# Optimization experiments

Measured on AMD Instinct MI355X. Metric: run time of the kernel, lower is better.

The kernel has to match this reference:

```python
import jax, jax.numpy as jnp
import numpy as np

HEADS = 4
HEAD_DIM = 32
IN_DIM = 128
N_TRIG = 48
N_SPAN = 128


def build_edges(T, S):
    # nodes are (trig r, span c) flattened row-major: n = r*S + c
    N = T * S
    nodes = jnp.arange(N, dtype=jnp.int32)
    r = nodes // S
    c = nodes % S
    # same-row neighbors (includes self loop once): [N, S]
    row_nb = r[:, None] * S + jnp.arange(S, dtype=jnp.int32)[None, :]
    # same-column neighbors excluding own row: [N, T-1]
    t_idx = jnp.arange(T - 1, dtype=jnp.int32)[None, :]
    t = t_idx + (t_idx >= r[:, None]).astype(jnp.int32)
    col_nb = t * S + c[:, None]
    deg = S + T - 1
    src = jnp.concatenate([row_nb, col_nb], axis=1).reshape(-1)  # [N*deg]
    dst = jnp.repeat(nodes, deg)
    return src, dst, N


def gat_conv(x, src, dst, N, W, att_src, att_dst, bias):
    # PyG GATConv (eval mode, dropout off), concat=True.
    # W: [in, H*Hd]; att_src/att_dst: [H, Hd]; bias: [H*Hd]
    h = (x @ W).reshape(N, HEADS, HEAD_DIM)          # [N,H,Hd]
    a_src = jnp.sum(h * att_src[None], axis=-1)      # [N,H]
    a_dst = jnp.sum(h * att_dst[None], axis=-1)      # [N,H]
    e = jax.nn.leaky_relu(a_src[src] + a_dst[dst], negative_slope=0.2)  # [E,H]
    # scatter-softmax over incoming edges per destination node
    m = jax.ops.segment_max(e, dst, num_segments=N)  # [N,H]
    ex = jnp.exp(e - m[dst])
    denom = jax.ops.segment_sum(ex, dst, num_segments=N)
    alpha = ex / denom[dst]                          # [E,H]
    msg = alpha[:, :, None] * h[src]                 # [E,H,Hd]
    out = jax.ops.segment_sum(msg, dst, num_segments=N)  # [N,H,Hd]
    return out.reshape(N, HEADS * HEAD_DIM) + bias[None]


def setup_inputs() -> dict:
    key = jax.random.key(0)
    ks = jax.random.split(key, 9)
    D = IN_DIM
    HD = HEADS * HEAD_DIM
    inp = {
        "pair_embeddings": jax.random.normal(ks[0], (1, N_TRIG, N_SPAN, D), dtype=jnp.float32),
        "W1": jax.random.normal(ks[1], (D, HD), dtype=jnp.float32) * (2.0 / (D + HD)) ** 0.5,
        "att_src1": jax.random.normal(ks[2], (HEADS, HEAD_DIM), dtype=jnp.float32) * 0.1,
        "att_dst1": jax.random.normal(ks[3], (HEADS, HEAD_DIM), dtype=jnp.float32) * 0.1,
        "b1": jnp.zeros((HD,), dtype=jnp.float32),
        "W2": jax.random.normal(ks[4], (HD, HD), dtype=jnp.float32) * (2.0 / (HD + HD)) ** 0.5,
        "att_src2": jax.random.normal(ks[5], (HEADS, HEAD_DIM), dtype=jnp.float32) * 0.1,
        "att_dst2": jax.random.normal(ks[6], (HEADS, HEAD_DIM), dtype=jnp.float32) * 0.1,
        "b2": jnp.zeros((HD,), dtype=jnp.float32),
        "num_trigs_kept": N_TRIG,
        "num_arg_spans_kept": N_SPAN,
    }
    return inp


def reference(pair_embeddings, W1, att_src1, att_dst1, b1, W2, att_src2, att_dst2, b2, num_trigs_kept, num_arg_spans_kept):
    T, S = int(num_trigs_kept), int(num_arg_spans_kept)
    src, dst, N = build_edges(T, S)
    # batch_size == 1: slice and flatten node features
    x = pair_embeddings[0, :T, :S].reshape(N, -1)
    x = jax.nn.elu(gat_conv(x, src, dst, N, W1, att_src1, att_dst1, b1))
    x = jax.nn.elu(gat_conv(x, src, dst, N, W2, att_src2, att_dst2, b2))
    return x
```

## Files before the change

kernel.cpp:

```cpp
#include <hip/hip_runtime.h>

#define T_TRIG 48
#define S_SPAN 128
#define NN (T_TRIG * S_SPAN)
#define D 128
#define DEG (S_SPAN + T_TRIG - 1)

__global__ __launch_bounds__(256) void gemm_att_kernel(
    const float* __restrict__ X, const float* __restrict__ W,
    const float* __restrict__ att_s, const float* __restrict__ att_d,
    float* __restrict__ H, float* __restrict__ asrc, float* __restrict__ adst)
{
    __shared__ float wl[128 * 128];
    const int tid = threadIdx.x;
    {
        const float4* W4 = (const float4*)W;
        float4* wl4 = (float4*)wl;
        #pragma unroll
        for (int i = 0; i < 16; ++i)
            wl4[tid + i * 256] = W4[tid + i * 256];
    }
    __syncthreads();

    const int tx = tid & 15;
    const int ty = tid >> 4;
    const int i0 = blockIdx.x * 32 + ty * 2;
    const int j0 = tx * 8;

    float acc[2][8];
    #pragma unroll
    for (int a = 0; a < 2; ++a)
        #pragma unroll
        for (int b = 0; b < 8; ++b) acc[a][b] = 0.f;

    const float* x0 = X + i0 * D;
    for (int k = 0; k < D; k += 4) {
        float4 xa4 = *(const float4*)(x0 + k);
        float4 xb4 = *(const float4*)(x0 + D + k);
        float xa[4] = {xa4.x, xa4.y, xa4.z, xa4.w};
        float xb[4] = {xb4.x, xb4.y, xb4.z, xb4.w};
        #pragma unroll
        for (int kk = 0; kk < 4; ++kk) {
            const float* wr = &wl[(k + kk) * 128 + j0];
            float4 w0 = *(const float4*)(wr);
            float4 w1 = *(const float4*)(wr + 4);
            float wv[8] = {w0.x, w0.y, w0.z, w0.w, w1.x, w1.y, w1.z, w1.w};
            #pragma unroll
            for (int jj = 0; jj < 8; ++jj) {
                acc[0][jj] = fmaf(xa[kk], wv[jj], acc[0][jj]);
                acc[1][jj] = fmaf(xb[kk], wv[jj], acc[1][jj]);
            }
        }
    }

    #pragma unroll
    for (int ii = 0; ii < 2; ++ii) {
        float4 o0 = {acc[ii][0], acc[ii][1], acc[ii][2], acc[ii][3]};
        float4 o1 = {acc[ii][4], acc[ii][5], acc[ii][6], acc[ii][7]};
        *(float4*)&H[(i0 + ii) * D + j0]     = o0;
        *(float4*)&H[(i0 + ii) * D + j0 + 4] = o1;
    }

    const int head = tx >> 2;
    const int dbase = head * 32 + (tx & 3) * 8;
    float asv[8], adv[8];
    #pragma unroll
    for (int jj = 0; jj < 8; ++jj) {
        asv[jj] = att_s[dbase + jj];
        adv[jj] = att_d[dbase + jj];
    }
    #pragma unroll
    for (int ii = 0; ii < 2; ++ii) {
        float ps = 0.f, pd = 0.f;
        #pragma unroll
        for (int jj = 0; jj < 8; ++jj) {
            ps = fmaf(acc[ii][jj], asv[jj], ps);
            pd = fmaf(acc[ii][jj], adv[jj], pd);
        }
        ps += __shfl_xor(ps, 1); ps += __shfl_xor(ps, 2);
        pd += __shfl_xor(pd, 1); pd += __shfl_xor(pd, 2);
        if ((tx & 3) == 0) {
            asrc[(i0 + ii) * 4 + head] = ps;
            adst[(i0 + ii) * 4 + head] = pd;
        }
    }
}

__global__ __launch_bounds__(128) void agg_kernel(
    const float* __restrict__ H, const float4* __restrict__ asrc4,
    const float4* __restrict__ adst4, const float* __restrict__ bias,
    float* __restrict__ out)
{
    __shared__ float w[DEG + 1][4];
    __shared__ float inv_den[4];

    const int tid = threadIdx.x;
    const int n = blockIdx.x;
    const int r = n >> 7;
    const int c = n & 127;

    const float4 ad = adst4[n];
    for (int j = tid; j < DEG; j += 128) {
        int src;
        if (j < 128) {
            src = (r << 7) + j;
        } else {
            int t = j - 128;
            t += (t >= r) ? 1 : 0;
            src = (t << 7) + c;
        }
        float4 as = asrc4[src];
        float e0 = as.x + ad.x; e0 = e0 > 0.f ? e0 : 0.2f * e0;
        float e1 = as.y + ad.y; e1 = e1 > 0.f ? e1 : 0.2f * e1;
        float e2 = as.z + ad.z; e2 = e2 > 0.f ? e2 : 0.2f * e2;
        float e3 = as.w + ad.w; e3 = e3 > 0.f ? e3 : 0.2f * e3;
        float4 ev = {e0, e1, e2, e3};
        *(float4*)&w[j][0] = ev;
    }
    __syncthreads();

    {
        const int head = tid >> 5;
        const int l = tid & 31;
        float m = -1e30f;
        for (int j = l; j < DEG; j += 32) m = fmaxf(m, w[j][head]);
        #pragma unroll
        for (int o = 16; o > 0; o >>= 1) m = fmaxf(m, __shfl_xor(m, o));
        float s = 0.f;
        for (int j = l; j < DEG; j += 32) {
            float v = __expf(w[j][head] - m);
            w[j][head] = v;
            s += v;
        }
        #pragma unroll
        for (int o = 16; o > 0; o >>= 1) s += __shfl_xor(s, o);
        if (l == 0) inv_den[head] = 1.f / s;
    }
    __syncthreads();

    const int f = tid;
    const int head = tid >> 5;
    float acc = 0.f;

    const float* hrow = H + (r << 7) * D + f;
    #pragma unroll 8
    for (int j = 0; j < S_SPAN; ++j)
        acc = fmaf(w[j][head], hrow[j * D], acc);

    const float* hcol = H + c * D + f;
    #pragma unroll 4
    for (int j2 = 0; j2 < T_TRIG - 1; ++j2) {
        int t = j2 + ((j2 >= r) ? 1 : 0);
        acc = fmaf(w[128 + j2][head], hcol[t * (S_SPAN * D)], acc);
    }

    acc = acc * inv_den[head] + bias[f];
    out[n * D + f] = acc > 0.f ? acc : (__expf(acc) - 1.f);
}

extern "C" void kernel_launch(void* const* d_in, const int* in_sizes, int n_in,
                              void* d_out, int out_size, void* d_ws, size_t ws_size,
                              hipStream_t stream)
{
    const float* pe  = (const float*)d_in[0];
    const float* W1  = (const float*)d_in[1];
    const float* as1 = (const float*)d_in[2];
    const float* ad1 = (const float*)d_in[3];
    const float* b1  = (const float*)d_in[4];
    const float* W2  = (const float*)d_in[5];
    const float* as2 = (const float*)d_in[6];
    const float* ad2 = (const float*)d_in[7];
    const float* b2  = (const float*)d_in[8];
    float* out = (float*)d_out;

    char* ws = (char*)d_ws;
    float* H    = (float*)(ws);
    float* X2   = (float*)(ws + (size_t)NN * D * 4);
    float* asrc = (float*)(ws + (size_t)2 * NN * D * 4);
    float* adst = (float*)(ws + (size_t)2 * NN * D * 4 + (size_t)NN * 4 * 4);

    gemm_att_kernel<<<dim3(NN / 32), dim3(256), 0, stream>>>(pe, W1, as1, ad1, H, asrc, adst);
    agg_kernel<<<dim3(NN), dim3(128), 0, stream>>>(H, (const float4*)asrc, (const float4*)adst, b1, X2);
    gemm_att_kernel<<<dim3(NN / 32), dim3(256), 0, stream>>>(X2, W2, as2, ad2, H, asrc, adst);
    agg_kernel<<<dim3(NN), dim3(128), 0, stream>>>(H, (const float4*)asrc, (const float4*)adst, b2, out);
}
```

Baseline: 84.23 us.

## Split GAT aggregation into row and column kernels sharing tiles in LDS

Replaces the per-node aggregation kernel with a row kernel (one block per trigger row and head) and a column kernel (one block per span column). Each stages its H tile once in shared memory and reuses it across all destination nodes, instead of re-gathering neighbor features per node. The softmax drops max-subtraction and combines unnormalized row and column partial sums, which risks exp overflow for large logits. The GEMM also stops staging W in LDS and reads it directly from global memory. The extra partial-numerator buffer adds global traffic.

```diff
diff --git a/kernel.cpp b/kernel.cpp
--- a/kernel.cpp
+++ b/kernel.cpp
@@ -4,24 +4,13 @@
 #define S_SPAN 128
 #define NN (T_TRIG * S_SPAN)
 #define D 128
-#define DEG (S_SPAN + T_TRIG - 1)
 
 __global__ __launch_bounds__(256) void gemm_att_kernel(
     const float* __restrict__ X, const float* __restrict__ W,
     const float* __restrict__ att_s, const float* __restrict__ att_d,
     float* __restrict__ H, float* __restrict__ asrc, float* __restrict__ adst)
 {
-    __shared__ float wl[128 * 128];
     const int tid = threadIdx.x;
-    {
-        const float4* W4 = (const float4*)W;
-        float4* wl4 = (float4*)wl;
-        #pragma unroll
-        for (int i = 0; i < 16; ++i)
-            wl4[tid + i * 256] = W4[tid + i * 256];
-    }
-    __syncthreads();
-
     const int tx = tid & 15;
     const int ty = tid >> 4;
     const int i0 = blockIdx.x * 32 + ty * 2;
@@ -33,7 +22,8 @@
         #pragma unroll
         for (int b = 0; b < 8; ++b) acc[a][b] = 0.f;
 
-    const float* x0 = X + i0 * D;
+    const float* x0 = X + (size_t)i0 * D;
+    #pragma unroll 4
     for (int k = 0; k < D; k += 4) {
         float4 xa4 = *(const float4*)(x0 + k);
         float4 xb4 = *(const float4*)(x0 + D + k);
@@ -41,7 +31,7 @@
         float xb[4] = {xb4.x, xb4.y, xb4.z, xb4.w};
         #pragma unroll
         for (int kk = 0; kk < 4; ++kk) {
-            const float* wr = &wl[(k + kk) * 128 + j0];
+            const float* wr = W + (k + kk) * D + j0;
             float4 w0 = *(const float4*)(wr);
             float4 w1 = *(const float4*)(wr + 4);
             float wv[8] = {w0.x, w0.y, w0.z, w0.w, w1.x, w1.y, w1.z, w1.w};
@@ -57,8 +47,8 @@
     for (int ii = 0; ii < 2; ++ii) {
         float4 o0 = {acc[ii][0], acc[ii][1], acc[ii][2], acc[ii][3]};
         float4 o1 = {acc[ii][4], acc[ii][5], acc[ii][6], acc[ii][7]};
-        *(float4*)&H[(i0 + ii) * D + j0]     = o0;
-        *(float4*)&H[(i0 + ii) * D + j0 + 4] = o1;
+        *(float4*)&H[(size_t)(i0 + ii) * D + j0]     = o0;
+        *(float4*)&H[(size_t)(i0 + ii) * D + j0 + 4] = o1;
     }
 
     const int head = tx >> 2;
@@ -86,76 +76,138 @@
     }
 }
 
-__global__ __launch_bounds__(128) void agg_kernel(
-    const float* __restrict__ H, const float4* __restrict__ asrc4,
-    const float4* __restrict__ adst4, const float* __restrict__ bias,
+__global__ __launch_bounds__(256) void row_agg_kernel(
+    const float* __restrict__ H, const float* __restrict__ asrc,
+    const float* __restrict__ adst, float* __restrict__ num_row,
+    float* __restrict__ den_row)
+{
+    __shared__ float sh_h[S_SPAN][32];
+    __shared__ float sh_as[S_SPAN];
+    const int tid = threadIdx.x;
+    const int r = blockIdx.x >> 2;
+    const int h = blockIdx.x & 3;
+    const int base = r * S_SPAN;
+
+    #pragma unroll
+    for (int it = 0; it < 4; ++it) {
+        int chunk = tid + it * 256;
+        int cp = chunk >> 3, fc = chunk & 7;
+        *(float4*)&sh_h[cp][fc * 4] =
+            *(const float4*)&H[(size_t)(base + cp) * D + h * 32 + fc * 4];
+    }
+    if (tid < S_SPAN) sh_as[tid] = asrc[(base + tid) * 4 + h];
+    __syncthreads();
+
+    const int fg = tid & 3;
+    const int cth = tid >> 2;
+    const float ad0 = adst[(base + cth) * 4 + h];
+    const float ad1 = adst[(base + cth + 64) * 4 + h];
+    float4 n00 = {0,0,0,0}, n01 = {0,0,0,0}, n10 = {0,0,0,0}, n11 = {0,0,0,0};
+    float den0 = 0.f, den1 = 0.f;
+
+    #pragma unroll 2
+    for (int cp = 0; cp < S_SPAN; ++cp) {
+        float a = sh_as[cp];
+        float4 h0 = *(float4*)&sh_h[cp][fg * 8];
+        float4 h1 = *(float4*)&sh_h[cp][fg * 8 + 4];
+        float e0 = a + ad0; e0 = fmaxf(e0, 0.2f * e0);
+        float e1 = a + ad1; e1 = fmaxf(e1, 0.2f * e1);
+        float w0 = __expf(e0);
+        float w1 = __expf(e1);
+        den0 += w0; den1 += w1;
+        n00.x = fmaf(w0, h0.x, n00.x); n00.y = fmaf(w0, h0.y, n00.y);
+        n00.z = fmaf(w0, h0.z, n00.z); n00.w = fmaf(w0, h0.w, n00.w);
+        n01.x = fmaf(w0, h1.x, n01.x); n01.y = fmaf(w0, h1.y, n01.y);
+        n01.z = fmaf(w0, h1.z, n01.z); n01.w = fmaf(w0, h1.w, n01.w);
+        n10.x = fmaf(w1, h0.x, n10.x); n10.y = fmaf(w1, h0.y, n10.y);
+        n10.z = fmaf(w1, h0.z, n10.z); n10.w = fmaf(w1, h0.w, n10.w);
+        n11.x = fmaf(w1, h1.x, n11.x); n11.y = fmaf(w1, h1.y, n11.y);
+        n11.z = fmaf(w1, h1.z, n11.z); n11.w = fmaf(w1, h1.w, n11.w);
+    }
+
+    const int n0 = base + cth, n1 = n0 + 64;
+    *(float4*)&num_row[(size_t)n0 * D + h * 32 + fg * 8]     = n00;
+    *(float4*)&num_row[(size_t)n0 * D + h * 32 + fg * 8 + 4] = n01;
+    *(float4*)&num_row[(size_t)n1 * D + h * 32 + fg * 8]     = n10;
+    *(float4*)&num_row[(size_t)n1 * D + h * 32 + fg * 8 + 4] = n11;
+    if (fg == 0) {
+        den_row[n0 * 4 + h] = den0;
+        den_row[n1 * 4 + h] = den1;
+    }
+}
+
+__global__ __launch_bounds__(256) void col_agg_kernel(
+    const float* __restrict__ H, const float* __restrict__ asrc,
+    const float* __restrict__ adst, const float* __restrict__ num_row,
+    const float* __restrict__ den_row, const float* __restrict__ bias,
     float* __restrict__ out)
 {
-    __shared__ float w[DEG + 1][4];
-    __shared__ float inv_den[4];
-
+    __shared__ float sh_h[T_TRIG][D];
+    __shared__ float sh_as[4][T_TRIG];
+    const int c = blockIdx.x;
     const int tid = threadIdx.x;
-    const int n = blockIdx.x;
-    const int r = n >> 7;
-    const int c = n & 127;
-
-    const float4 ad = adst4[n];
-    for (int j = tid; j < DEG; j += 128) {
-        int src;
-        if (j < 128) {
-            src = (r << 7) + j;
-        } else {
-            int t = j - 128;
-            t += (t >= r) ? 1 : 0;
-            src = (t << 7) + c;
-        }
-        float4 as = asrc4[src];
-        float e0 = as.x + ad.x; e0 = e0 > 0.f ? e0 : 0.2f * e0;
-        float e1 = as.y + ad.y; e1 = e1 > 0.f ? e1 : 0.2f * e1;
-        float e2 = as.z + ad.z; e2 = e2 > 0.f ? e2 : 0.2f * e2;
-        float e3 = as.w + ad.w; e3 = e3 > 0.f ? e3 : 0.2f * e3;
-        float4 ev = {e0, e1, e2, e3};
-        *(float4*)&w[j][0] = ev;
+
+    #pragma unroll
+    for (int it = 0; it < 6; ++it) {
+        int chunk = tid + it * 256;
+        int t = chunk >> 5, fc = chunk & 31;
+        *(float4*)&sh_h[t][fc * 4] =
+            *(const float4*)&H[(size_t)(t * S_SPAN + c) * D + fc * 4];
+    }
+    if (tid < 4 * T_TRIG) {
+        int hh = tid / T_TRIG, t = tid - hh * T_TRIG;
+        sh_as[hh][t] = asrc[(t * S_SPAN + c) * 4 + hh];
     }
     __syncthreads();
 
-    {
-        const int head = tid >> 5;
-        const int l = tid & 31;
-        float m = -1e30f;
-        for (int j = l; j < DEG; j += 32) m = fmaxf(m, w[j][head]);
-        #pragma unroll
-        for (int o = 16; o > 0; o >>= 1) m = fmaxf(m, __shfl_xor(m, o));
-        float s = 0.f;
-        for (int j = l; j < DEG; j += 32) {
-            float v = __expf(w[j][head] - m);
-            w[j][head] = v;
-            s += v;
-        }
-        #pragma unroll
-        for (int o = 16; o > 0; o >>= 1) s += __shfl_xor(s, o);
-        if (l == 0) inv_den[head] = 1.f / s;
-    }
-    __syncthreads();
-
-    const int f = tid;
-    const int head = tid >> 5;
-    float acc = 0.f;
-
-    const float* hrow = H + (r << 7) * D + f;
-    #pragma unroll 8
-    for (int j = 0; j < S_SPAN; ++j)
-        acc = fmaf(w[j][head], hrow[j * D], acc);
-
-    const float* hcol = H + c * D + f;
-    #pragma unroll 4
-    for (int j2 = 0; j2 < T_TRIG - 1; ++j2) {
-        int t = j2 + ((j2 >= r) ? 1 : 0);
-        acc = fmaf(w[128 + j2][head], hcol[t * (S_SPAN * D)], acc);
-    }
-
-    acc = acc * inv_den[head] + bias[f];
-    out[n * D + f] = acc > 0.f ? acc : (__expf(acc) - 1.f);
+    const int f4g = tid & 31;
+    const int tg = tid >> 5;
+    const int head = f4g >> 3;
+
+    float4 num[6];
+    float den[6], ad[6];
+    #pragma unroll
+    for (int dd = 0; dd < 6; ++dd) {
+        num[dd] = {0,0,0,0};
+        den[dd] = 0.f;
+        ad[dd] = adst[((tg * 6 + dd) * S_SPAN + c) * 4 + head];
+    }
+
+    for (int tp = 0; tp < T_TRIG; ++tp) {
+        float a = sh_as[head][tp];
+        float4 hv = *(float4*)&sh_h[tp][f4g * 4];
+        #pragma unroll
+        for (int dd = 0; dd < 6; ++dd) {
+            float e = a + ad[dd];
+            e = fmaxf(e, 0.2f * e);
+            float w = __expf(e);
+            w = (tp == tg * 6 + dd) ? 0.f : w;
+            den[dd] += w;
+            num[dd].x = fmaf(w, hv.x, num[dd].x);
+            num[dd].y = fmaf(w, hv.y, num[dd].y);
+            num[dd].z = fmaf(w, hv.z, num[dd].z);
+            num[dd].w = fmaf(w, hv.w, num[dd].w);
+        }
+    }
+
+    const float4 b4 = *(const float4*)&bias[f4g * 4];
+    #pragma unroll
+    for (int dd = 0; dd < 6; ++dd) {
+        int n = (tg * 6 + dd) * S_SPAN + c;
+        float4 nr = *(const float4*)&num_row[(size_t)n * D + f4g * 4];
+        float dr = den_row[n * 4 + head];
+        float inv = 1.f / (dr + den[dd]);
+        float4 o;
+        o.x = (nr.x + num[dd].x) * inv + b4.x;
+        o.y = (nr.y + num[dd].y) * inv + b4.y;
+        o.z = (nr.z + num[dd].z) * inv + b4.z;
+        o.w = (nr.w + num[dd].w) * inv + b4.w;
+        o.x = o.x > 0.f ? o.x : (__expf(o.x) - 1.f);
+        o.y = o.y > 0.f ? o.y : (__expf(o.y) - 1.f);
+        o.z = o.z > 0.f ? o.z : (__expf(o.z) - 1.f);
+        o.w = o.w > 0.f ? o.w : (__expf(o.w) - 1.f);
+        *(float4*)&out[(size_t)n * D + f4g * 4] = o;
+    }
 }
 
 extern "C" void kernel_launch(void* const* d_in, const int* in_sizes, int n_in,
@@ -173,14 +225,18 @@
     const float* b2  = (const float*)d_in[8];
     float* out = (float*)d_out;
 
-    char* ws = (char*)d_ws;
-    float* H    = (float*)(ws);
-    float* X2   = (float*)(ws + (size_t)NN * D * 4);
-    float* asrc = (float*)(ws + (size_t)2 * NN * D * 4);
-    float* adst = (float*)(ws + (size_t)2 * NN * D * 4 + (size_t)NN * 4 * 4);
-
-    gemm_att_kernel<<<dim3(NN / 32), dim3(256), 0, stream>>>(pe, W1, as1, ad1, H, asrc, adst);
-    agg_kernel<<<dim3(NN), dim3(128), 0, stream>>>(H, (const float4*)asrc, (const float4*)adst, b1, X2);
-    gemm_att_kernel<<<dim3(NN / 32), dim3(256), 0, stream>>>(X2, W2, as2, ad2, H, asrc, adst);
-    agg_kernel<<<dim3(NN), dim3(128), 0, stream>>>(H, (const float4*)asrc, (const float4*)adst, b2, out);
-}
+    float* ws = (float*)d_ws;
+    float* H     = ws;
+    float* X2    = H + (size_t)NN * D;
+    float* numr  = X2 + (size_t)NN * D;
+    float* asrcb = numr + (size_t)NN * D;
+    float* adstb = asrcb + (size_t)NN * 4;
+    float* denb  = adstb + (size_t)NN * 4;
+
+    gemm_att_kernel<<<dim3(NN / 32), dim3(256), 0, stream>>>(pe, W1, as1, ad1, H, asrcb, adstb);
+    row_agg_kernel<<<dim3(T_TRIG * 4), dim3(256), 0, stream>>>(H, asrcb, adstb, numr, denb);
+    col_agg_kernel<<<dim3(S_SPAN), dim3(256), 0, stream>>>(H, asrcb, adstb, numr, denb, b1, X2);
+    gemm_att_kernel<<<dim3(NN / 32), dim3(256), 0, stream>>>(X2, W2, as2, ad2, H, asrcb, adstb);
+    row_agg_kernel<<<dim3(T_TRIG * 4), dim3(256), 0, stream>>>(H, asrcb, adstb, numr, denb);
+    col_agg_kernel<<<dim3(S_SPAN), dim3(256), 0, stream>>>(H, asrcb, adstb, numr, denb, b2, out);
+}
```

After: 93.97 us. 11.6% more time.
